# Kernel optimization log

Measured on AMD Instinct MI355X. Metric: run time of the kernel, lower is better.

## Reference

```python
import jax, jax.numpy as jnp
import numpy as np

NNZ = 1_000_000
M = N = 8192
K = 128

def setup_inputs() -> dict:
    key = jax.random.key(0)
    k1, k2, k3, k4, k5 = jax.random.split(key, 5)
    mask_vals = jax.random.normal(k1, (NNZ,), dtype=jnp.float32)
    rows = jax.random.randint(k2, (NNZ,), 0, M, dtype=jnp.int64)
    cols = jax.random.randint(k3, (NNZ,), 0, N, dtype=jnp.int64)
    mat1 = jax.random.normal(k4, (M, K), dtype=jnp.float32)
    mat2 = jax.random.normal(k5, (K, N), dtype=jnp.float32)
    return {"mask_vals": mask_vals, "rows": rows, "cols": cols,
            "mat1": mat1, "mat2": mat2}

def reference(mask_vals, rows, cols, mat1, mat2):
    # torch.sparse.sampled_addmm with alpha=beta=1:
    # out.values = mask.values + (mat1 @ mat2)[rows, cols]
    # SDDMM: only compute the dot products at the sampled (row, col) pairs.
    a = mat1[rows]        # [nnz, K] gather of mat1 rows
    b = mat2[:, cols].T   # [nnz, K] gather of mat2 cols
    sampled = jnp.einsum('nk,nk->n', a, b)  # per-nnz dot product
    return mask_vals + sampled
```

## Files before the change

kernel.cpp:

```cpp
#include <hip/hip_runtime.h>
#include <hip/hip_fp16.h>


#define KDIM 128
#define BATCH 4

typedef _Float16 half2v __attribute__((ext_vector_type(2)));

union F4H8 {
  float4 f4;
  half2v h2[4];
  _Float16 h[8];
};

__global__ __launch_bounds__(256) void convert_f16_kernel(
    const float* __restrict__ in, _Float16* __restrict__ out, int n) {
  int i = (blockIdx.x * 256 + threadIdx.x) * 8;
  if (i >= n) return;
  const float4* p = (const float4*)(in + i);
  float4 x0 = p[0];
  float4 x1 = p[1];
  F4H8 o;
  o.h[0] = (_Float16)x0.x; o.h[1] = (_Float16)x0.y;
  o.h[2] = (_Float16)x0.z; o.h[3] = (_Float16)x0.w;
  o.h[4] = (_Float16)x1.x; o.h[5] = (_Float16)x1.y;
  o.h[6] = (_Float16)x1.z; o.h[7] = (_Float16)x1.w;
  *(float4*)(out + i) = o.f4;
}

__global__ __launch_bounds__(256) void transpose_f16_kernel(
    const float* __restrict__ in, _Float16* __restrict__ out, int N) {
  __shared__ float tile[32][33];
  int bx = blockIdx.x * 32;
  int by = blockIdx.y * 32;
  int tx = threadIdx.x;
  int ty = threadIdx.y;
#pragma unroll
  for (int j = 0; j < 32; j += 8) {
    tile[ty + j][tx] = in[(size_t)(by + ty + j) * N + (bx + tx)];
  }
  __syncthreads();
#pragma unroll
  for (int j = 0; j < 32; j += 8) {
    out[(size_t)(bx + ty + j) * KDIM + (by + tx)] = (_Float16)tile[tx][ty + j];
  }
}

__device__ __forceinline__ float dot8(const F4H8& a, const F4H8& b) {
  float s = 0.f;
#if __has_builtin(__builtin_amdgcn_fdot2)
#pragma unroll
  for (int j = 0; j < 4; ++j) s = __builtin_amdgcn_fdot2(a.h2[j], b.h2[j], s, false);
#else
#pragma unroll
  for (int j = 0; j < 8; ++j) s += (float)a.h[j] * (float)b.h[j];
#endif
  return s;
}

__device__ __forceinline__ float red16(float s) {
  s += __shfl_xor(s, 8);
  s += __shfl_xor(s, 4);
  s += __shfl_xor(s, 2);
  s += __shfl_xor(s, 1);
  return s;
}

__global__ __launch_bounds__(256) void sddmm_f16_b4_kernel(
    const float* __restrict__ mask_vals,
    const int* __restrict__ rows,
    const int* __restrict__ cols,
    const _Float16* __restrict__ m1,
    const _Float16* __restrict__ m2t,
    float* __restrict__ out, int nnz) {
  int tid = blockIdx.x * 256 + threadIdx.x;
  int grp = tid >> 4;
  int lane = tid & 15;
  int g0 = grp * BATCH;
  if (g0 >= nnz) return;

  if (g0 + BATCH <= nnz) {
    int4 r4 = *(const int4*)(rows + g0);
    int4 c4 = *(const int4*)(cols + g0);

    F4H8 a0, a1, a2, a3, b0, b1, b2, b3;
    a0.f4 = ((const float4*)(m1 + (size_t)r4.x * KDIM))[lane];
    a1.f4 = ((const float4*)(m1 + (size_t)r4.y * KDIM))[lane];
    a2.f4 = ((const float4*)(m1 + (size_t)r4.z * KDIM))[lane];
    a3.f4 = ((const float4*)(m1 + (size_t)r4.w * KDIM))[lane];
    b0.f4 = ((const float4*)(m2t + (size_t)c4.x * KDIM))[lane];
    b1.f4 = ((const float4*)(m2t + (size_t)c4.y * KDIM))[lane];
    b2.f4 = ((const float4*)(m2t + (size_t)c4.z * KDIM))[lane];
    b3.f4 = ((const float4*)(m2t + (size_t)c4.w * KDIM))[lane];

    float s0 = dot8(a0, b0);
    float s1 = dot8(a1, b1);
    float s2 = dot8(a2, b2);
    float s3 = dot8(a3, b3);

    s0 = red16(s0);
    s1 = red16(s1);
    s2 = red16(s2);
    s3 = red16(s3);

    if (lane == 0) {
      float4 mv = *(const float4*)(mask_vals + g0);
      float4 o;
      o.x = mv.x + s0;
      o.y = mv.y + s1;
      o.z = mv.z + s2;
      o.w = mv.w + s3;
      *(float4*)(out + g0) = o;
    }
  } else {
    for (int g = g0; g < nnz; ++g) {
      int r = rows[g];
      int c = cols[g];
      F4H8 a, b;
      a.f4 = ((const float4*)(m1 + (size_t)r * KDIM))[lane];
      b.f4 = ((const float4*)(m2t + (size_t)c * KDIM))[lane];
      float s = red16(dot8(a, b));
      if (lane == 0) out[g] = mask_vals[g] + s;
    }
  }
}

__global__ __launch_bounds__(256) void sddmm16_strided_kernel(
    const float* __restrict__ mask_vals,
    const int* __restrict__ rows,
    const int* __restrict__ cols,
    const float* __restrict__ mat1,
    const float* __restrict__ mat2,
    float* __restrict__ out, int nnz, int N) {
  int tid = blockIdx.x * 256 + threadIdx.x;
  int g = tid >> 4;
  int lane = tid & 15;
  if (g >= nnz) return;
  int r = rows[g];
  int c = cols[g];
  const float* arow = mat1 + (size_t)r * KDIM;
  float s = 0.f;
#pragma unroll
  for (int j = 0; j < 8; ++j) {
    int k = lane + 16 * j;
    s += arow[k] * mat2[(size_t)k * N + c];
  }
  s = red16(s);
  if (lane == 0) out[g] = mask_vals[g] + s;
}

extern "C" void kernel_launch(void* const* d_in, const int* in_sizes, int n_in,
                              void* d_out, int out_size, void* d_ws, size_t ws_size,
                              hipStream_t stream) {
  const float* mask_vals = (const float*)d_in[0];
  const int*   rows      = (const int*)d_in[1];
  const int*   cols      = (const int*)d_in[2];
  const float* mat1      = (const float*)d_in[3];
  const float* mat2      = (const float*)d_in[4];
  float*       out       = (float*)d_out;

  int nnz   = in_sizes[0];
  int m1_sz = in_sizes[3];
  int N     = in_sizes[4] / KDIM;

  size_t need = (size_t)m1_sz * sizeof(_Float16)
              + (size_t)KDIM * N * sizeof(_Float16);
  if (ws_size >= need) {
    _Float16* m1h  = (_Float16*)d_ws;
    _Float16* m2th = m1h + m1_sz;

    convert_f16_kernel<<<(m1_sz / 8 + 255) / 256, 256, 0, stream>>>(
        mat1, m1h, m1_sz);
    dim3 tb(32, 8);
    dim3 tg(N / 32, KDIM / 32);
    transpose_f16_kernel<<<tg, tb, 0, stream>>>(mat2, m2th, N);

    int groups = (nnz + BATCH - 1) / BATCH;
    int blocks = (groups * 16 + 255) / 256;
    sddmm_f16_b4_kernel<<<blocks, 256, 0, stream>>>(mask_vals, rows, cols,
                                                    m1h, m2th, out, nnz);
  } else {
    int blocks = (nnz * 16 + 255) / 256;
    sddmm16_strided_kernel<<<blocks, 256, 0, stream>>>(mask_vals, rows, cols,
                                                       mat1, mat2, out, nnz, N);
  }
}
```

Measured before the change: 100.8 us.

## Bucket nonzeros by column slab and stage mat2 slab in shared memory

Adds a counting-sort pipeline (histogram, column scan, base offsets, scatter) that groups nonzeros into 64 buckets of 128 columns each. A new slab kernel loads the 128x128 fp16 slice of transposed mat2 for one bucket into LDS, so B-operand gathers come from shared memory instead of random global reads, and results are written back through stored original indices. The cost is four extra kernel launches, a full extra pass that writes the sorted row/col, mask and index arrays, and scattered output writes. The path runs only when N is 8192 and the workspace is large enough; otherwise it falls back to the previous kernels.

```diff
diff --git a/kernel.cpp b/kernel.cpp
--- a/kernel.cpp
+++ b/kernel.cpp
@@ -3,7 +3,10 @@
 
 
 #define KDIM 128
-#define BATCH 4
+#define NBUCK 64
+#define SLAB_COLS 128
+#define NBLK 512
+#define SUBS 16
 
 typedef _Float16 half2v __attribute__((ext_vector_type(2)));
 
@@ -12,6 +15,7 @@
   half2v h2[4];
   _Float16 h[8];
 };
+
 
 __global__ __launch_bounds__(256) void convert_f16_kernel(
     const float* __restrict__ in, _Float16* __restrict__ out, int n) {
@@ -46,6 +50,82 @@
   }
 }
 
+
+__global__ __launch_bounds__(256) void hist_kernel(
+    const int* __restrict__ cols, int nnz, int epb,
+    int* __restrict__ blockHist) {
+  __shared__ int h[NBUCK];
+  if (threadIdx.x < NBUCK) h[threadIdx.x] = 0;
+  __syncthreads();
+  int lo = blockIdx.x * epb;
+  int hi = min(lo + epb, nnz);
+  for (int i = lo + threadIdx.x; i < hi; i += 256) {
+    atomicAdd(&h[cols[i] >> 7], 1);
+  }
+  __syncthreads();
+  if (threadIdx.x < NBUCK) {
+    blockHist[blockIdx.x * NBUCK + threadIdx.x] = h[threadIdx.x];
+  }
+}
+
+__global__ __launch_bounds__(NBLK) void colscan_kernel(
+    const int* __restrict__ blockHist, int* __restrict__ blockScan,
+    int* __restrict__ totals) {
+  __shared__ int sh[NBLK];
+  int b = blockIdx.x;
+  int t = threadIdx.x;
+  int v = blockHist[t * NBUCK + b];
+  sh[t] = v;
+  __syncthreads();
+  for (int off = 1; off < NBLK; off <<= 1) {
+    int x = (t >= off) ? sh[t - off] : 0;
+    __syncthreads();
+    sh[t] += x;
+    __syncthreads();
+  }
+  blockScan[t * NBUCK + b] = sh[t] - v;
+  if (t == NBLK - 1) totals[b] = sh[t];
+}
+
+__global__ __launch_bounds__(64) void base_kernel(
+    const int* __restrict__ totals, int* __restrict__ bucketBase) {
+  if (threadIdx.x == 0) {
+    int acc = 0;
+    for (int b = 0; b < NBUCK; ++b) {
+      bucketBase[b] = acc;
+      acc += totals[b];
+      acc = (acc + 7) & ~7;
+    }
+    bucketBase[NBUCK] = acc;
+  }
+}
+
+__global__ __launch_bounds__(256) void scatter_kernel(
+    const int* __restrict__ rows, const int* __restrict__ cols,
+    const float* __restrict__ mask, int nnz, int epb,
+    const int* __restrict__ blockScan, const int* __restrict__ bucketBase,
+    int* __restrict__ sortedRC, float* __restrict__ sortedMask,
+    int* __restrict__ sortedIdx) {
+  __shared__ int h[NBUCK];
+  if (threadIdx.x < NBUCK) h[threadIdx.x] = 0;
+  __syncthreads();
+  int blk = blockIdx.x;
+  int lo = blk * epb;
+  int hi = min(lo + epb, nnz);
+  for (int i = lo + threadIdx.x; i < hi; i += 256) {
+    int c = cols[i];
+    int r = rows[i];
+    float mv = mask[i];
+    int b = c >> 7;
+    int rank = atomicAdd(&h[b], 1);
+    int pos = bucketBase[b] + blockScan[blk * NBUCK + b] + rank;
+    sortedRC[pos] = (r << 16) | c;
+    sortedMask[pos] = mv;
+    sortedIdx[pos] = i;
+  }
+}
+
+
 __device__ __forceinline__ float dot8(const F4H8& a, const F4H8& b) {
   float s = 0.f;
 #if __has_builtin(__builtin_amdgcn_fdot2)
@@ -66,23 +146,92 @@
   return s;
 }
 
-__global__ __launch_bounds__(256) void sddmm_f16_b4_kernel(
-    const float* __restrict__ mask_vals,
-    const int* __restrict__ rows,
-    const int* __restrict__ cols,
+__global__ __launch_bounds__(512) void sddmm_slab_kernel(
     const _Float16* __restrict__ m1,
     const _Float16* __restrict__ m2t,
-    float* __restrict__ out, int nnz) {
+    const int* __restrict__ sortedRC,
+    const float* __restrict__ sortedMask,
+    const int* __restrict__ sortedIdx,
+    const int* __restrict__ bucketBase,
+    const int* __restrict__ totals,
+    float* __restrict__ out) {
+  __shared__ _Float16 slab[SLAB_COLS * KDIM];
+  int s = blockIdx.x / SUBS;
+  int sub = blockIdx.x % SUBS;
+
+  {
+    const float4* src = (const float4*)(m2t + (size_t)s * SLAB_COLS * KDIM);
+    float4* dst = (float4*)slab;
+#pragma unroll
+    for (int i = 0; i < (SLAB_COLS * KDIM / 8) / 512; ++i) {
+      dst[threadIdx.x + i * 512] = src[threadIdx.x + i * 512];
+    }
+  }
+  __syncthreads();
+
+  int start = bucketBase[s];
+  int cnt = totals[s];
+  int hi0 = start + cnt;
+  int per = ((cnt + SUBS - 1) / SUBS + 3) & ~3;
+  int lo = start + sub * per;
+  int hi = min(lo + per, hi0);
+
+  int grp = threadIdx.x >> 4;
+  int lane = threadIdx.x & 15;
+
+  for (int g0 = lo + grp * 4; g0 < hi; g0 += 32 * 4) {
+    if (g0 + 4 <= hi) {
+      int4 rc4 = *(const int4*)(sortedRC + g0);
+      float4 mv4 = *(const float4*)(sortedMask + g0);
+      int4 idx4 = *(const int4*)(sortedIdx + g0);
+
+      F4H8 a0, a1, a2, a3, b0, b1, b2, b3;
+      a0.f4 = ((const float4*)(m1 + (size_t)(rc4.x >> 16) * KDIM))[lane];
+      a1.f4 = ((const float4*)(m1 + (size_t)(rc4.y >> 16) * KDIM))[lane];
+      a2.f4 = ((const float4*)(m1 + (size_t)(rc4.z >> 16) * KDIM))[lane];
+      a3.f4 = ((const float4*)(m1 + (size_t)(rc4.w >> 16) * KDIM))[lane];
+      b0.f4 = ((const float4*)(slab + (rc4.x & (SLAB_COLS - 1)) * KDIM))[lane];
+      b1.f4 = ((const float4*)(slab + (rc4.y & (SLAB_COLS - 1)) * KDIM))[lane];
+      b2.f4 = ((const float4*)(slab + (rc4.z & (SLAB_COLS - 1)) * KDIM))[lane];
+      b3.f4 = ((const float4*)(slab + (rc4.w & (SLAB_COLS - 1)) * KDIM))[lane];
+
+      float s0 = red16(dot8(a0, b0));
+      float s1 = red16(dot8(a1, b1));
+      float s2 = red16(dot8(a2, b2));
+      float s3 = red16(dot8(a3, b3));
+
+      if (lane == 0) {
+        out[idx4.x] = mv4.x + s0;
+        out[idx4.y] = mv4.y + s1;
+        out[idx4.z] = mv4.z + s2;
+        out[idx4.w] = mv4.w + s3;
+      }
+    } else {
+      for (int g = g0; g < hi; ++g) {
+        int rc = sortedRC[g];
+        F4H8 a, b;
+        a.f4 = ((const float4*)(m1 + (size_t)(rc >> 16) * KDIM))[lane];
+        b.f4 = ((const float4*)(slab + (rc & (SLAB_COLS - 1)) * KDIM))[lane];
+        float sv = red16(dot8(a, b));
+        if (lane == 0) out[sortedIdx[g]] = sortedMask[g] + sv;
+      }
+    }
+  }
+}
+
+
+__global__ __launch_bounds__(256) void sddmm_f16_b4_kernel(
+    const float* __restrict__ mask_vals, const int* __restrict__ rows,
+    const int* __restrict__ cols, const _Float16* __restrict__ m1,
+    const _Float16* __restrict__ m2t, float* __restrict__ out, int nnz) {
   int tid = blockIdx.x * 256 + threadIdx.x;
   int grp = tid >> 4;
   int lane = tid & 15;
-  int g0 = grp * BATCH;
+  int g0 = grp * 4;
   if (g0 >= nnz) return;
-
-  if (g0 + BATCH <= nnz) {
+  if (g0 + 4 <= nnz) {
     int4 r4 = *(const int4*)(rows + g0);
     int4 c4 = *(const int4*)(cols + g0);
-
     F4H8 a0, a1, a2, a3, b0, b1, b2, b3;
     a0.f4 = ((const float4*)(m1 + (size_t)r4.x * KDIM))[lane];
     a1.f4 = ((const float4*)(m1 + (size_t)r4.y * KDIM))[lane];
@@ -92,46 +241,30 @@
     b1.f4 = ((const float4*)(m2t + (size_t)c4.y * KDIM))[lane];
     b2.f4 = ((const float4*)(m2t + (size_t)c4.z * KDIM))[lane];
     b3.f4 = ((const float4*)(m2t + (size_t)c4.w * KDIM))[lane];
-
-    float s0 = dot8(a0, b0);
-    float s1 = dot8(a1, b1);
-    float s2 = dot8(a2, b2);
-    float s3 = dot8(a3, b3);
-
-    s0 = red16(s0);
-    s1 = red16(s1);
-    s2 = red16(s2);
-    s3 = red16(s3);
-
+    float s0 = red16(dot8(a0, b0));
+    float s1 = red16(dot8(a1, b1));
+    float s2 = red16(dot8(a2, b2));
+    float s3 = red16(dot8(a3, b3));
     if (lane == 0) {
       float4 mv = *(const float4*)(mask_vals + g0);
-      float4 o;
-      o.x = mv.x + s0;
-      o.y = mv.y + s1;
-      o.z = mv.z + s2;
-      o.w = mv.w + s3;
+      float4 o = {mv.x + s0, mv.y + s1, mv.z + s2, mv.w + s3};
       *(float4*)(out + g0) = o;
     }
   } else {
     for (int g = g0; g < nnz; ++g) {
-      int r = rows[g];
-      int c = cols[g];
       F4H8 a, b;
-      a.f4 = ((const float4*)(m1 + (size_t)r * KDIM))[lane];
-      b.f4 = ((const float4*)(m2t + (size_t)c * KDIM))[lane];
-      float s = red16(dot8(a, b));
-      if (lane == 0) out[g] = mask_vals[g] + s;
+      a.f4 = ((const float4*)(m1 + (size_t)rows[g] * KDIM))[lane];
+      b.f4 = ((const float4*)(m2t + (size_t)cols[g] * KDIM))[lane];
+      float sv = red16(dot8(a, b));
+      if (lane == 0) out[g] = mask_vals[g] + sv;
     }
   }
 }
 
 __global__ __launch_bounds__(256) void sddmm16_strided_kernel(
-    const float* __restrict__ mask_vals,
-    const int* __restrict__ rows,
-    const int* __restrict__ cols,
-    const float* __restrict__ mat1,
-    const float* __restrict__ mat2,
-    float* __restrict__ out, int nnz, int N) {
+    const float* __restrict__ mask_vals, const int* __restrict__ rows,
+    const int* __restrict__ cols, const float* __restrict__ mat1,
+    const float* __restrict__ mat2, float* __restrict__ out, int nnz, int N) {
   int tid = blockIdx.x * 256 + threadIdx.x;
   int g = tid >> 4;
   int lane = tid & 15;
@@ -148,6 +281,7 @@
   s = red16(s);
   if (lane == 0) out[g] = mask_vals[g] + s;
 }
+
 
 extern "C" void kernel_launch(void* const* d_in, const int* in_sizes, int n_in,
                               void* d_out, int out_size, void* d_ws, size_t ws_size,
@@ -163,24 +297,60 @@
   int m1_sz = in_sizes[3];
   int N     = in_sizes[4] / KDIM;
 
-  size_t need = (size_t)m1_sz * sizeof(_Float16)
-              + (size_t)KDIM * N * sizeof(_Float16);
-  if (ws_size >= need) {
-    _Float16* m1h  = (_Float16*)d_ws;
-    _Float16* m2th = m1h + m1_sz;
-
-    convert_f16_kernel<<<(m1_sz / 8 + 255) / 256, 256, 0, stream>>>(
-        mat1, m1h, m1_sz);
+  auto align256 = [](size_t x) { return (x + 255) & ~(size_t)255; };
+  size_t off = 0;
+  size_t o_m1h   = off; off = align256(off + (size_t)m1_sz * 2);
+  size_t o_m2th  = off; off = align256(off + (size_t)KDIM * N * 2);
+  size_t cap     = (size_t)nnz + 8 * NBUCK + 64;
+  size_t o_rc    = off; off = align256(off + cap * 4);
+  size_t o_mk    = off; off = align256(off + cap * 4);
+  size_t o_ix    = off; off = align256(off + cap * 4);
+  size_t o_bh    = off; off = align256(off + (size_t)NBLK * NBUCK * 4);
+  size_t o_bs    = off; off = align256(off + (size_t)NBLK * NBUCK * 4);
+  size_t o_tot   = off; off = align256(off + NBUCK * 4);
+  size_t o_base  = off; off = align256(off + (NBUCK + 1) * 4);
+  size_t need_full = off;
+  size_t need_min  = align256((size_t)m1_sz * 2) + align256((size_t)KDIM * N * 2);
+
+  char* ws = (char*)d_ws;
+
+  if (ws_size >= need_full && N == 8192) {
+    _Float16* m1h   = (_Float16*)(ws + o_m1h);
+    _Float16* m2th  = (_Float16*)(ws + o_m2th);
+    int*      sRC   = (int*)(ws + o_rc);
+    float*    sMK   = (float*)(ws + o_mk);
+    int*      sIX   = (int*)(ws + o_ix);
+    int*      bh    = (int*)(ws + o_bh);
+    int*      bs    = (int*)(ws + o_bs);
+    int*      tot   = (int*)(ws + o_tot);
+    int*      bbase = (int*)(ws + o_base);
+
+    convert_f16_kernel<<<(m1_sz / 8 + 255) / 256, 256, 0, stream>>>(mat1, m1h, m1_sz);
     dim3 tb(32, 8);
     dim3 tg(N / 32, KDIM / 32);
     transpose_f16_kernel<<<tg, tb, 0, stream>>>(mat2, m2th, N);
 
-    int groups = (nnz + BATCH - 1) / BATCH;
+    int epb = (nnz + NBLK - 1) / NBLK;
+    hist_kernel<<<NBLK, 256, 0, stream>>>(cols, nnz, epb, bh);
+    colscan_kernel<<<NBUCK, NBLK, 0, stream>>>(bh, bs, tot);
+    base_kernel<<<1, 64, 0, stream>>>(tot, bbase);
+    scatter_kernel<<<NBLK, 256, 0, stream>>>(rows, cols, mask_vals, nnz, epb,
+                                             bs, bbase, sRC, sMK, sIX);
+    sddmm_slab_kernel<<<NBUCK * SUBS, 512, 0, stream>>>(m1h, m2th, sRC, sMK,
+                                                        sIX, bbase, tot, out);
+  } else if (ws_size >= need_min) {
+    _Float16* m1h  = (_Float16*)ws;
+    _Float16* m2th = m1h + m1_sz;
+    convert_f16_kernel<<<(m1_sz / 8 + 255) / 256, 256, 0, stream>>>(mat1, m1h, m1_sz);
+    dim3 tb(32, 8);
+    dim3 tg(N / 32, KDIM / 32);
+    transpose_f16_kernel<<<tg, tb, 0, stream>>>(mat2, m2th, N);
+    int groups = (nnz + 3) / 4;
     int blocks = (groups * 16 + 255) / 256;
-    sddmm_f16_b4_kernel<<<blocks, 256, 0, stream>>>(mask_vals, rows, cols,
-                                                    m1h, m2th, out, nnz);
+    sddmm_f16_b4_kernel<<<blocks, 256, 0, stream>>>(mask_vals, rows, cols, m1h,
+                                                    m2th, out, nnz);
   } else {
-    int blocks = (nnz * 16 + 255) / 256;
+    int blocks = ((size_t)nnz * 16 + 255) / 256;
     sddmm16_strided_kernel<<<blocks, 256, 0, stream>>>(mask_vals, rows, cols,
                                                        mat1, mat2, out, nnz, N);
   }
```

New measurement: 122.6 us. 1.22x slower.
